# Performance work log

Measured on AMD Instinct MI355X. Metric: run time of the kernel, lower is better.

The kernel has to match this reference:

```python
import jax, jax.numpy as jnp
import numpy as np

DIM = 1024
HEADS = 16
DIM_HEAD = 64
INNER = HEADS * DIM_HEAD
SCALE = DIM_HEAD ** -0.5


def rotate_half(t):
    # '... (j d) -> ... j d' with j=2: split last dim in half
    x1, x2 = jnp.split(t, 2, axis=-1)
    return jnp.concatenate((-x2, x1), axis=-1)


def rotary_pos(n, d, dtype):
    inv_freq = 1.0 / (10000.0 ** (jnp.arange(0, d, 2, dtype=jnp.float32) / d))
    freqs = jnp.arange(n, dtype=jnp.float32)[:, None] * inv_freq[None, :]  # (n, d/2)
    return jnp.concatenate((freqs, freqs), axis=-1).astype(dtype)  # (n, d)


def apply_rope(pos, t):
    return t * jnp.cos(pos) + rotate_half(t) * jnp.sin(pos)


def setup_inputs() -> dict:
    key = jax.random.key(0)
    ks = jax.random.split(key, 5)
    x = jax.random.normal(ks[0], (2, 2048, DIM), dtype=jnp.float32)
    gamma = jnp.ones((DIM,), dtype=jnp.float32)
    beta = jnp.zeros((DIM,), dtype=jnp.float32)
    Wq = jax.random.normal(ks[1], (DIM, INNER), dtype=jnp.float32) * 0.02
    Wkv = jax.random.normal(ks[2], (DIM, 2 * INNER), dtype=jnp.float32) * 0.02
    Wo = jax.random.normal(ks[3], (INNER, DIM), dtype=jnp.float32) * 0.02
    return {"x": x, "gamma": gamma, "beta": beta, "Wq": Wq, "Wkv": Wkv, "Wo": Wo}


def reference(x, gamma, beta, Wq, Wkv, Wo):
    b, n, _ = x.shape
    # LayerNorm with learned gamma, fixed-zero beta buffer
    mu = jnp.mean(x, axis=-1, keepdims=True)
    var = jnp.var(x, axis=-1, keepdims=True)
    xn = (x - mu) / jnp.sqrt(var + 1e-5) * gamma + beta

    q = xn @ Wq                       # (b, n, inner)
    kv = xn @ Wkv
    k, v = jnp.split(kv, 2, axis=-1)

    def to_heads(t):
        return t.reshape(b, n, HEADS, DIM_HEAD).transpose(0, 2, 1, 3)  # b h n d

    q, k, v = map(to_heads, (q, k, v))

    pos = rotary_pos(n, DIM_HEAD, x.dtype)  # (n, d)
    q = apply_rope(pos, q)
    k = apply_rope(pos, k)

    q = q * SCALE
    sim = jnp.einsum('bhid,bhjd->bhij', q, k)

    neg = -jnp.finfo(sim.dtype).max
    causal_mask = jnp.triu(jnp.ones((n, n), dtype=bool), k=1)
    sim = jnp.where(causal_mask, neg, sim)

    attn = jax.nn.softmax(sim, axis=-1)
    out = jnp.einsum('bhij,bhjd->bhid', attn, v)
    out = out.transpose(0, 2, 1, 3).reshape(b, n, INNER)
    return out @ Wo
```

## Files before the change

kernel.cpp:

```cpp
#include <hip/hip_runtime.h>
#include <stdint.h>

typedef unsigned short u16;
typedef __attribute__((ext_vector_type(8))) short short8;
typedef __attribute__((ext_vector_type(4))) float floatx4;
typedef __attribute__((ext_vector_type(4))) unsigned short u16x4;
typedef __attribute__((ext_vector_type(2))) unsigned int uint2v;

__device__ __forceinline__ float bf2f(u16 v) {
  union { uint32_t u; float f; } x; x.u = ((uint32_t)v) << 16; return x.f;
}
__device__ __forceinline__ u16 f2bf(float f) {
  union { float f; uint32_t u; } x; x.f = f;
  uint32_t r = x.u + 0x7fffu + ((x.u >> 16) & 1u);
  return (u16)(r >> 16);
}
__device__ __forceinline__ uint32_t fu(float f) {
  union { float f; uint32_t u; } x; x.f = f; return x.u;
}

#define GL2LDS(g, l)                                                          \
  __builtin_amdgcn_global_load_lds(                                           \
      (const __attribute__((address_space(1))) void*)(g),                     \
      (__attribute__((address_space(3))) void*)(l), 16, 0, 0)

#define WAITBAR(N)                                                            \
  asm volatile("s_waitcnt vmcnt(" #N ")\n\ts_barrier" ::: "memory")

__global__ __launch_bounds__(256) void prep_k(const float* __restrict__ x,
                                              const float* __restrict__ gamma,
                                              const float* __restrict__ beta,
                                              const float* __restrict__ Wq,
                                              const float* __restrict__ Wkv,
                                              const float* __restrict__ Wo,
                                              u16* __restrict__ xn,
                                              u16* __restrict__ wqkvT,
                                              u16* __restrict__ woT) {
  int bid = blockIdx.x;
  int t = threadIdx.x;
  if (bid < 4096) {
    int row = bid;
    const float* xr = x + (size_t)row * 1024;
    float4 xv = *(const float4*)(xr + t * 4);
    float v0 = xv.x, v1 = xv.y, v2 = xv.z, v3 = xv.w;
    float s = v0 + v1 + v2 + v3;
    float s2 = v0 * v0 + v1 * v1 + v2 * v2 + v3 * v3;
#pragma unroll
    for (int d = 1; d < 64; d <<= 1) {
      s += __shfl_xor(s, d, 64);
      s2 += __shfl_xor(s2, d, 64);
    }
    __shared__ float red[8];
    int lane = t & 63, wv = t >> 6;
    if (lane == 0) { red[wv] = s; red[4 + wv] = s2; }
    __syncthreads();
    s = red[0] + red[1] + red[2] + red[3];
    s2 = red[4] + red[5] + red[6] + red[7];
    float mu = s * (1.0f / 1024.0f);
    float var = s2 * (1.0f / 1024.0f) - mu * mu;
    float rstd = rsqrtf(var + 1e-5f);
    float4 gv = *(const float4*)(gamma + t * 4);
    float4 bv = *(const float4*)(beta + t * 4);
    u16x4 ov;
    ov.x = f2bf((v0 - mu) * rstd * gv.x + bv.x);
    ov.y = f2bf((v1 - mu) * rstd * gv.y + bv.y);
    ov.z = f2bf((v2 - mu) * rstd * gv.z + bv.z);
    ov.w = f2bf((v3 - mu) * rstd * gv.w + bv.w);
    *(u16x4*)(xn + (size_t)row * 1024 + t * 4) = ov;
  } else {
    __shared__ float tile[32][33];
    int wb = bid - 4096;
    const float* in;
    u16* outp;
    int C;
    if (wb < 1024) { in = Wq; outp = wqkvT; C = 1024; }
    else if (wb < 3072) { wb -= 1024; in = Wkv; outp = wqkvT + 1024 * 1024; C = 2048; }
    else { wb -= 3072; in = Wo; outp = woT; C = 1024; }
    int nbx = C >> 5;
    int c0 = (wb % nbx) * 32, r0 = (wb / nbx) * 32;
    int tx = t & 31, ty = t >> 5;
#pragma unroll
    for (int i = 0; i < 32; i += 8)
      tile[ty + i][tx] = in[(size_t)(r0 + ty + i) * C + c0 + tx];
    __syncthreads();
#pragma unroll
    for (int i = 0; i < 32; i += 8)
      outp[(size_t)(c0 + ty + i) * 1024 + r0 + tx] = f2bf(tile[tx][ty + i]);
  }
}

__global__ __launch_bounds__(256) void gemm_qkv_k(const u16* __restrict__ A,
                                                  const u16* __restrict__ BT,
                                                  u16* __restrict__ C) {
  const int K = 1024, lda = 1024, ldc = 3072;
  __shared__ __align__(16) u16 lA[3][128 * 32];
  __shared__ __align__(16) u16 lB[3][128 * 32];
  int tid = threadIdx.x;
  int bm = blockIdx.y * 128;
  int bn = blockIdx.x * 128;
  int w = tid >> 6, l = tid & 63;
  int wm = (w >> 1) * 64, wn = (w & 1) * 64;
  int lr = l & 15, lq = l >> 4;
  floatx4 acc[4][4] = {};
  int sr = w * 16 + (l >> 2);
  int sc = (l & 3) * 8;
  int sds = sr * 32 + sc;
  const u16* pA0 = A + (size_t)(bm + sr) * lda + sc;
  const u16* pA1 = pA0 + (size_t)64 * lda;
  const u16* pB0 = BT + (size_t)(bn + sr) * K + sc;
  const u16* pB1 = pB0 + (size_t)64 * K;
  int ao[4], bo[4];
#pragma unroll
  for (int i = 0; i < 4; i++) {
    ao[i] = (wm + i * 16 + lr) * 32 + lq * 8;
    bo[i] = (wn + i * 16 + lr) * 32 + lq * 8;
  }

#define STAGE_QKV(bi)                                                         \
  {                                                                           \
    GL2LDS(pA0, &lA[bi][sds]);                                                \
    GL2LDS(pA1, &lA[bi][sds + 2048]);                                         \
    GL2LDS(pB0, &lB[bi][sds]);                                                \
    GL2LDS(pB1, &lB[bi][sds + 2048]);                                         \
    pA0 += 32; pA1 += 32; pB0 += 32; pB1 += 32;                               \
  }
#define COMPUTE_QKV(bi)                                                       \
  {                                                                           \
    short8 afr[4], bfr[4];                                                    \
    _Pragma("unroll") for (int i = 0; i < 4; i++)                             \
        afr[i] = *(const short8*)(&lA[bi][ao[i]]);                            \
    _Pragma("unroll") for (int i = 0; i < 4; i++)                             \
        bfr[i] = *(const short8*)(&lB[bi][bo[i]]);                            \
    _Pragma("unroll") for (int mi = 0; mi < 4; mi++)                          \
        _Pragma("unroll") for (int ni = 0; ni < 4; ni++)                      \
            acc[mi][ni] = __builtin_amdgcn_mfma_f32_16x16x32_bf16(            \
                afr[mi], bfr[ni], acc[mi][ni], 0, 0, 0);                      \
  }

  STAGE_QKV(0);
  STAGE_QKV(1);
#pragma unroll 1
  for (int t = 0; t < 10; ++t) {
    WAITBAR(4); STAGE_QKV(2); COMPUTE_QKV(0);
    WAITBAR(4); STAGE_QKV(0); COMPUTE_QKV(1);
    WAITBAR(4); STAGE_QKV(1); COMPUTE_QKV(2);
  }
  WAITBAR(4); COMPUTE_QKV(0);
  WAITBAR(0); COMPUTE_QKV(1);

  int sec = bn >> 10;
  if (sec == 2) {
#pragma unroll
    for (int mi = 0; mi < 4; mi++)
#pragma unroll
      for (int ni = 0; ni < 4; ni++) {
        int col = bn + wn + ni * 16 + lr;
        int cv = col - 2048;
        int row = bm + wm + mi * 16 + lq * 4;
        int bq = row >> 11;
        int n = row & 2047;
        int bh = (bq << 4) | (cv >> 6);
        int d = cv & 63;
        size_t L = ((size_t)(bh * 64 + d) << 11) + n;
        u16x4 ov;
        ov.x = f2bf(acc[mi][ni][0]);
        ov.y = f2bf(acc[mi][ni][1]);
        ov.z = f2bf(acc[mi][ni][2]);
        ov.w = f2bf(acc[mi][ni][3]);
        *(u16x4*)(C + (L >> 10) * 3072 + 2048 + (L & 1023)) = ov;
      }
  } else {
    float QS = (sec == 0) ? 0.125f * 1.44269504088896f : 1.0f;
#pragma unroll
    for (int ni = 0; ni < 2; ni++) {
      int i = ni * 16 + lr;
      float invf = exp2f(-(float)i * 0.4152410118609203f);
#pragma unroll
      for (int mi = 0; mi < 4; mi++)
#pragma unroll
        for (int r = 0; r < 4; r++) {
          int row = bm + wm + mi * 16 + lq * 4 + r;
          int n = row & 2047;
          float ang = (float)n * invf;
          float s_, c_;
          __sincosf(ang, &s_, &c_);
          float x1 = acc[mi][ni][r], x2 = acc[mi][ni + 2][r];
          int col = bn + wn + ni * 16 + lr;
          C[(size_t)row * ldc + col] = f2bf((x1 * c_ - x2 * s_) * QS);
          C[(size_t)row * ldc + col + 32] = f2bf((x2 * c_ + x1 * s_) * QS);
        }
    }
  }
}

__global__ __launch_bounds__(256) void gemm64_bf16_k(const u16* __restrict__ A,
                                                     const u16* __restrict__ BT,
                                                     float* __restrict__ C,
                                                     int K, int lda, int ldc) {
  __shared__ __align__(16) u16 lA[3][64 * 32];
  __shared__ __align__(16) u16 lB[3][128 * 32];
  int tid = threadIdx.x;
  int bm = blockIdx.y * 64;
  int bn = blockIdx.x * 128;
  int w = tid >> 6, l = tid & 63;
  int wm = (w >> 1) * 32, wn = (w & 1) * 64;
  int lr = l & 15, lq = l >> 4;
  floatx4 acc[2][4] = {};
  int sr = w * 16 + (l >> 2);
  int sc = (l & 3) * 8;
  int sds = sr * 32 + sc;
  const u16* pA0 = A + (size_t)(bm + sr) * lda + sc;
  const u16* pB0 = BT + (size_t)(bn + sr) * K + sc;
  const u16* pB1 = pB0 + (size_t)64 * K;
  int ao[2], bo[4];
#pragma unroll
  for (int i = 0; i < 2; i++) ao[i] = (wm + i * 16 + lr) * 32 + lq * 8;
#pragma unroll
  for (int i = 0; i < 4; i++) bo[i] = (wn + i * 16 + lr) * 32 + lq * 8;

#define STAGE_O(bi)                                                           \
  {                                                                           \
    GL2LDS(pA0, &lA[bi][sds]);                                                \
    GL2LDS(pB0, &lB[bi][sds]);                                                \
    GL2LDS(pB1, &lB[bi][sds + 2048]);                                         \
    pA0 += 32; pB0 += 32; pB1 += 32;                                          \
  }
#define COMPUTE_O(bi)                                                         \
  {                                                                           \
    short8 afr[2], bfr[4];                                                    \
    _Pragma("unroll") for (int i = 0; i < 2; i++)                             \
        afr[i] = *(const short8*)(&lA[bi][ao[i]]);                            \
    _Pragma("unroll") for (int i = 0; i < 4; i++)                             \
        bfr[i] = *(const short8*)(&lB[bi][bo[i]]);                            \
    _Pragma("unroll") for (int mi = 0; mi < 2; mi++)                          \
        _Pragma("unroll") for (int ni = 0; ni < 4; ni++)                      \
            acc[mi][ni] = __builtin_amdgcn_mfma_f32_16x16x32_bf16(            \
                afr[mi], bfr[ni], acc[mi][ni], 0, 0, 0);                      \
  }

  STAGE_O(0);
  STAGE_O(1);
#pragma unroll 1
  for (int t = 0; t < 10; ++t) {
    WAITBAR(3); STAGE_O(2); COMPUTE_O(0);
    WAITBAR(3); STAGE_O(0); COMPUTE_O(1);
    WAITBAR(3); STAGE_O(1); COMPUTE_O(2);
  }
  WAITBAR(3); COMPUTE_O(0);
  WAITBAR(0); COMPUTE_O(1);

#pragma unroll
  for (int mi = 0; mi < 2; mi++)
#pragma unroll
    for (int ni = 0; ni < 4; ni++)
#pragma unroll
      for (int r = 0; r < 4; r++) {
        int row = bm + wm + mi * 16 + lq * 4 + r;
        int col = bn + wn + ni * 16 + lr;
        C[(size_t)row * ldc + col] = acc[mi][ni][r];
      }
}

#define LPT 64
#define FIXM 4.0f
__device__ __forceinline__ void attn_tile2(const u16* lK, const u16* lV, u16* lp,
                                           const short8* aq, floatx4* o,
                                           float& l_i, int lr, int lq,
                                           bool diag, int q0, int k0g,
                                           short8 ones) {
  floatx4 s[4];
#pragma unroll
  for (int ni = 0; ni < 4; ni++) {
    floatx4 a = {};
#pragma unroll
    for (int kc = 0; kc < 2; kc++) {
      int R = ni * 16 + lr;
      int c8 = (kc * 4 + lq) ^ (R & 7);
      short8 kf = *(const short8*)&lK[R * 64 + c8 * 8];
      a = __builtin_amdgcn_mfma_f32_16x16x32_bf16(kf, aq[kc], a, 0, 0, 0);
    }
    s[ni] = a;
  }
  if (diag) {
    int qg = q0 + lr;
#pragma unroll
    for (int ni = 0; ni < 4; ni++)
#pragma unroll
      for (int r = 0; r < 4; r++) {
        int kg = k0g + ni * 16 + lq * 4 + r;
        if (kg > qg) s[ni][r] = -1e30f;
      }
  }
  int swz = (lr & 7) << 3;
#pragma unroll
  for (int ni = 0; ni < 4; ni++) {
    float p0 = exp2f(s[ni][0] - FIXM), p1 = exp2f(s[ni][1] - FIXM);
    float p2 = exp2f(s[ni][2] - FIXM), p3 = exp2f(s[ni][3] - FIXM);
    uint2v dw;
    dw.x = __builtin_amdgcn_perm(fu(p1), fu(p0), 0x07060302u);
    dw.y = __builtin_amdgcn_perm(fu(p3), fu(p2), 0x07060302u);
    *(uint2v*)&lp[lr * LPT + ((ni * 16 + lq * 4) ^ swz)] = dw;
  }
  short8 pb0 = *(const short8*)&lp[lr * LPT + ((lq * 8) ^ swz)];
  short8 pb1 = *(const short8*)&lp[lr * LPT + ((32 + lq * 8) ^ swz)];
  floatx4 z = {};
  z = __builtin_amdgcn_mfma_f32_16x16x32_bf16(ones, pb0, z, 0, 0, 0);
  z = __builtin_amdgcn_mfma_f32_16x16x32_bf16(ones, pb1, z, 0, 0, 0);
  l_i += z[0];
#pragma unroll
  for (int di = 0; di < 4; di++) {
    int R = di * 16 + lr;
    int c80 = lq ^ (R & 7);
    int c81 = (4 + lq) ^ (R & 7);
    short8 v0 = *(const short8*)&lV[R * 64 + c80 * 8];
    o[di] = __builtin_amdgcn_mfma_f32_16x16x32_bf16(v0, pb0, o[di], 0, 0, 0);
    short8 v1 = *(const short8*)&lV[R * 64 + c81 * 8];
    o[di] = __builtin_amdgcn_mfma_f32_16x16x32_bf16(v1, pb1, o[di], 0, 0, 0);
  }
}

__global__ __launch_bounds__(256) void attn_k(const u16* __restrict__ qkv,
                                              u16* __restrict__ out) {
  __shared__ __align__(16) u16 lK[2][64 * 64];
  __shared__ __align__(16) u16 lV[2][64 * 64];
  __shared__ __align__(16) u16 lP[4][16 * LPT];
  int bh = blockIdx.x;
  int b = bh >> 4, h = bh & 15;
  int y = blockIdx.y;
  int g = y >> 3, o_ = y & 7;
  int j = (g & 1) ? ((g << 3) + 7 - o_) : y;
  int tid = threadIdx.x;
  int w = tid >> 6, l = tid & 63;
  int lr = l & 15, lq = l >> 4;
  int q0 = j * 64 + w * 16;
  const u16* qb = qkv + (size_t)b * 2048 * 3072 + h * 64;
  const u16* kb = qkv + (size_t)b * 2048 * 3072 + 1024 + h * 64;
  int bh64 = bh * 64;
  short8 aq[2];
  aq[0] = *(const short8*)(qb + (size_t)(q0 + lr) * 3072 + lq * 8);
  aq[1] = *(const short8*)(qb + (size_t)(q0 + lr) * 3072 + 32 + lq * 8);
  short8 ones;
#pragma unroll
  for (int i = 0; i < 8; i++) ones[i] = (short)0x3F80;
  floatx4 o[4] = {};
  float l_ = 0.0f;
  int srow8 = l >> 3;
  int sc8 = (l & 7) ^ srow8;
  u16* lp = &lP[w][0];
  auto stage = [&](int bufi, int kt) {
#pragma unroll
    for (int c = 0; c < 2; c++) {
      int m = w + c * 4;
      int row = m * 8 + srow8;
      GL2LDS(kb + (size_t)(kt * 64 + row) * 3072 + sc8 * 8, &lK[bufi][m * 512]);
      int nn = kt * 64 + sc8 * 8;
      GL2LDS(qkv + (size_t)((bh64 + row) * 2 + (nn >> 10)) * 3072 + 2048 +
                 (nn & 1023),
             &lV[bufi][m * 512]);
    }
  };
  stage(0, 0);
  for (int kt = 0; kt <= j; ++kt) {
    int cur = kt & 1;
    __syncthreads();
    if (kt < j) stage(cur ^ 1, kt + 1);
    attn_tile2(lK[cur], lV[cur], lp, aq, o, l_, lr, lq, kt == j, q0, kt * 64,
               ones);
  }
  float rl = 1.0f / l_;
#pragma unroll
  for (int di = 0; di < 4; di++) {
    uint2v dw;
    u16 a0 = f2bf(o[di][0] * rl), a1 = f2bf(o[di][1] * rl);
    u16 a2 = f2bf(o[di][2] * rl), a3 = f2bf(o[di][3] * rl);
    dw.x = (uint32_t)a0 | ((uint32_t)a1 << 16);
    dw.y = (uint32_t)a2 | ((uint32_t)a3 << 16);
    int dcol = h * 64 + di * 16 + lq * 4;
    *(uint2v*)(out + ((size_t)(b * 2048 + q0 + lr)) * 1024 + dcol) = dw;
  }
}

extern "C" void kernel_launch(void* const* d_in, const int* in_sizes, int n_in,
                              void* d_out, int out_size, void* d_ws, size_t ws_size,
                              hipStream_t stream) {
  const float* x = (const float*)d_in[0];
  const float* gamma = (const float*)d_in[1];
  const float* beta = (const float*)d_in[2];
  const float* Wq = (const float*)d_in[3];
  const float* Wkv = (const float*)d_in[4];
  const float* Wo = (const float*)d_in[5];
  float* out = (float*)d_out;
  char* ws = (char*)d_ws;

  u16* qkv = (u16*)(ws);
  u16* wqkvT = (u16*)(ws + 25165824);
  u16* woT = (u16*)(ws + 31457280);
  u16* xn = (u16*)(ws + 33554432);
  u16* attn_out = xn;

  prep_k<<<8192, 256, 0, stream>>>(x, gamma, beta, Wq, Wkv, Wo, xn, wqkvT, woT);
  gemm_qkv_k<<<dim3(24, 32), 256, 0, stream>>>(xn, wqkvT, qkv);
  attn_k<<<dim3(32, 32), 256, 0, stream>>>(qkv, attn_out);
  gemm64_bf16_k<<<dim3(8, 64), 256, 0, stream>>>(attn_out, woT, out, 1024, 1024, 1024);
}
```

Measured before the change: 196.1 us.

## Retile QKV GEMM to 128x384 with 512 threads and load V directly to registers

```diff
diff --git a/kernel.cpp b/kernel.cpp
--- a/kernel.cpp
+++ b/kernel.cpp
@@ -26,6 +26,8 @@
 
 #define WAITBAR(N)                                                            \
   asm volatile("s_waitcnt vmcnt(" #N ")\n\ts_barrier" ::: "memory")
+#define BARX asm volatile("s_barrier" ::: "memory")
+#define VM0BARX asm volatile("s_waitcnt vmcnt(0)\n\ts_barrier" ::: "memory")
 
 __global__ __launch_bounds__(256) void prep_k(const float* __restrict__ x,
                                               const float* __restrict__ gamma,
@@ -89,106 +91,125 @@
   }
 }
 
-__global__ __launch_bounds__(256) void gemm_qkv_k(const u16* __restrict__ A,
-                                                  const u16* __restrict__ BT,
-                                                  u16* __restrict__ C) {
-  const int K = 1024, lda = 1024, ldc = 3072;
-  __shared__ __align__(16) u16 lA[3][128 * 32];
-  __shared__ __align__(16) u16 lB[3][128 * 32];
+__global__ __launch_bounds__(512, 1) void gemm_qkv_k(const u16* __restrict__ A,
+                                                     const u16* __restrict__ BT,
+                                                     u16* __restrict__ C) {
+  __shared__ __align__(16) u16 sA[2][128 * 64];
+  __shared__ __align__(16) u16 sB[2][384 * 64];
   int tid = threadIdx.x;
+  int w = tid >> 6, l = tid & 63;
+  int lr = l & 15, lq = l >> 4;
+  int wm = w >> 1, wn = w & 1;
   int bm = blockIdx.y * 128;
-  int bn = blockIdx.x * 128;
-  int w = tid >> 6, l = tid & 63;
-  int wm = (w >> 1) * 64, wn = (w & 1) * 64;
-  int lr = l & 15, lq = l >> 4;
-  floatx4 acc[4][4] = {};
-  int sr = w * 16 + (l >> 2);
-  int sc = (l & 3) * 8;
-  int sds = sr * 32 + sc;
-  const u16* pA0 = A + (size_t)(bm + sr) * lda + sc;
-  const u16* pA1 = pA0 + (size_t)64 * lda;
-  const u16* pB0 = BT + (size_t)(bn + sr) * K + sc;
-  const u16* pB1 = pB0 + (size_t)64 * K;
-  int ao[4], bo[4];
-#pragma unroll
-  for (int i = 0; i < 4; i++) {
-    ao[i] = (wm + i * 16 + lr) * 32 + lq * 8;
-    bo[i] = (wn + i * 16 + lr) * 32 + lq * 8;
-  }
-
-#define STAGE_QKV(bi)                                                         \
+  int bn = blockIdx.x * 384;
+  floatx4 acc[2][12] = {};
+  int gcol = ((tid & 7) ^ ((tid >> 3) & 7)) * 8;
+  int strow = tid >> 3;
+  int t8 = tid * 8;
+  const u16* gA = A + (size_t)(bm + strow) * 1024 + gcol;
+  const u16* gB = BT + (size_t)(bn + strow) * 1024 + gcol;
+  int csw = (lr & 7) << 3;
+  int ar = (wm * 32 + lr) * 64;
+  int br = (wn * 192 + lr) * 64;
+
+#define ST_A(bi)                                                              \
+  { GL2LDS(gA, &sA[bi][t8]); GL2LDS(gA + 65536, &sA[bi][t8 + 4096]); }
+#define ST_B(bi)                                                              \
+  { GL2LDS(gB, &sB[bi][t8]);                                                  \
+    GL2LDS(gB + 65536, &sB[bi][t8 + 4096]);                                   \
+    GL2LDS(gB + 131072, &sB[bi][t8 + 8192]);                                  \
+    GL2LDS(gB + 196608, &sB[bi][t8 + 12288]);                                 \
+    GL2LDS(gB + 262144, &sB[bi][t8 + 16384]);                                 \
+    GL2LDS(gB + 327680, &sB[bi][t8 + 20480]); }
+#define HALF(p, kh)                                                           \
   {                                                                           \
-    GL2LDS(pA0, &lA[bi][sds]);                                                \
-    GL2LDS(pA1, &lA[bi][sds + 2048]);                                         \
-    GL2LDS(pB0, &lB[bi][sds]);                                                \
-    GL2LDS(pB1, &lB[bi][sds + 2048]);                                         \
-    pA0 += 32; pA1 += 32; pB0 += 32; pB1 += 32;                               \
-  }
-#define COMPUTE_QKV(bi)                                                       \
+    int co_ = ((kh)*32 + lq * 8) ^ csw;                                       \
+    short8 a0_ = *(const short8*)&sA[p][ar + co_];                            \
+    short8 a1_ = *(const short8*)&sA[p][ar + 1024 + co_];                     \
+    _Pragma("unroll") for (int g = 0; g < 3; g++) {                           \
+      short8 b0_ = *(const short8*)&sB[p][br + (g * 4 + 0) * 1024 + co_];     \
+      short8 b1_ = *(const short8*)&sB[p][br + (g * 4 + 1) * 1024 + co_];     \
+      short8 b2_ = *(const short8*)&sB[p][br + (g * 4 + 2) * 1024 + co_];     \
+      short8 b3_ = *(const short8*)&sB[p][br + (g * 4 + 3) * 1024 + co_];     \
+      acc[0][g*4+0] = __builtin_amdgcn_mfma_f32_16x16x32_bf16(a0_, b0_, acc[0][g*4+0], 0, 0, 0); \
+      acc[1][g*4+0] = __builtin_amdgcn_mfma_f32_16x16x32_bf16(a1_, b0_, acc[1][g*4+0], 0, 0, 0); \
+      acc[0][g*4+1] = __builtin_amdgcn_mfma_f32_16x16x32_bf16(a0_, b1_, acc[0][g*4+1], 0, 0, 0); \
+      acc[1][g*4+1] = __builtin_amdgcn_mfma_f32_16x16x32_bf16(a1_, b1_, acc[1][g*4+1], 0, 0, 0); \
+      acc[0][g*4+2] = __builtin_amdgcn_mfma_f32_16x16x32_bf16(a0_, b2_, acc[0][g*4+2], 0, 0, 0); \
+      acc[1][g*4+2] = __builtin_amdgcn_mfma_f32_16x16x32_bf16(a1_, b2_, acc[1][g*4+2], 0, 0, 0); \
+      acc[0][g*4+3] = __builtin_amdgcn_mfma_f32_16x16x32_bf16(a0_, b3_, acc[0][g*4+3], 0, 0, 0); \
+      acc[1][g*4+3] = __builtin_amdgcn_mfma_f32_16x16x32_bf16(a1_, b3_, acc[1][g*4+3], 0, 0, 0); \
+    }                                                                         \
+  }
+#define KT(p, q, DOST)                                                        \
   {                                                                           \
-    short8 afr[4], bfr[4];                                                    \
-    _Pragma("unroll") for (int i = 0; i < 4; i++)                             \
-        afr[i] = *(const short8*)(&lA[bi][ao[i]]);                            \
-    _Pragma("unroll") for (int i = 0; i < 4; i++)                             \
-        bfr[i] = *(const short8*)(&lB[bi][bo[i]]);                            \
-    _Pragma("unroll") for (int mi = 0; mi < 4; mi++)                          \
-        _Pragma("unroll") for (int ni = 0; ni < 4; ni++)                      \
-            acc[mi][ni] = __builtin_amdgcn_mfma_f32_16x16x32_bf16(            \
-                afr[mi], bfr[ni], acc[mi][ni], 0, 0, 0);                      \
-  }
-
-  STAGE_QKV(0);
-  STAGE_QKV(1);
+    if (DOST) { ST_A(q); ST_B(q); gA += 64; gB += 64; }                       \
+    BARX; __builtin_amdgcn_s_setprio(1);                                      \
+    HALF(p, 0);                                                               \
+    __builtin_amdgcn_s_setprio(0); BARX;                                      \
+    __builtin_amdgcn_s_setprio(1);                                            \
+    HALF(p, 1);                                                               \
+    __builtin_amdgcn_s_setprio(0); VM0BARX;                                   \
+  }
+
+  ST_A(0); ST_B(0); gA += 64; gB += 64;
+  VM0BARX;
 #pragma unroll 1
-  for (int t = 0; t < 10; ++t) {
-    WAITBAR(4); STAGE_QKV(2); COMPUTE_QKV(0);
-    WAITBAR(4); STAGE_QKV(0); COMPUTE_QKV(1);
-    WAITBAR(4); STAGE_QKV(1); COMPUTE_QKV(2);
-  }
-  WAITBAR(4); COMPUTE_QKV(0);
-  WAITBAR(0); COMPUTE_QKV(1);
-
-  int sec = bn >> 10;
-  if (sec == 2) {
-#pragma unroll
-    for (int mi = 0; mi < 4; mi++)
-#pragma unroll
-      for (int ni = 0; ni < 4; ni++) {
-        int col = bn + wn + ni * 16 + lr;
+  for (int t = 0; t < 7; ++t) {
+    KT(0, 1, 1);
+    KT(1, 0, 1);
+  }
+  KT(0, 1, 1);
+  KT(1, 0, 0);
+
+#pragma unroll
+  for (int nig = 0; nig < 3; nig++) {
+    int col0 = bn + wn * 192 + nig * 64;
+    int sec = col0 >> 10;
+    if (sec == 2) {
+#pragma unroll
+      for (int p4 = 0; p4 < 4; p4++) {
+        int ni = nig * 4 + p4;
+        int col = col0 + p4 * 16 + lr;
         int cv = col - 2048;
-        int row = bm + wm + mi * 16 + lq * 4;
-        int bq = row >> 11;
-        int n = row & 2047;
-        int bh = (bq << 4) | (cv >> 6);
-        int d = cv & 63;
-        size_t L = ((size_t)(bh * 64 + d) << 11) + n;
-        u16x4 ov;
-        ov.x = f2bf(acc[mi][ni][0]);
-        ov.y = f2bf(acc[mi][ni][1]);
-        ov.z = f2bf(acc[mi][ni][2]);
-        ov.w = f2bf(acc[mi][ni][3]);
-        *(u16x4*)(C + (L >> 10) * 3072 + 2048 + (L & 1023)) = ov;
+#pragma unroll
+        for (int mi = 0; mi < 2; mi++) {
+          int row = bm + wm * 32 + mi * 16 + lq * 4;
+          int bq = row >> 11;
+          int n = row & 2047;
+          int bh = (bq << 4) | (cv >> 6);
+          int d = cv & 63;
+          size_t L = ((size_t)(bh * 64 + d) << 11) + n;
+          u16x4 ov;
+          ov.x = f2bf(acc[mi][ni][0]);
+          ov.y = f2bf(acc[mi][ni][1]);
+          ov.z = f2bf(acc[mi][ni][2]);
+          ov.w = f2bf(acc[mi][ni][3]);
+          *(u16x4*)(C + (L >> 10) * 3072 + 2048 + (L & 1023)) = ov;
+        }
       }
-  } else {
-    float QS = (sec == 0) ? 0.125f * 1.44269504088896f : 1.0f;
-#pragma unroll
-    for (int ni = 0; ni < 2; ni++) {
-      int i = ni * 16 + lr;
-      float invf = exp2f(-(float)i * 0.4152410118609203f);
-#pragma unroll
-      for (int mi = 0; mi < 4; mi++)
-#pragma unroll
-        for (int r = 0; r < 4; r++) {
-          int row = bm + wm + mi * 16 + lq * 4 + r;
-          int n = row & 2047;
-          float ang = (float)n * invf;
-          float s_, c_;
-          __sincosf(ang, &s_, &c_);
-          float x1 = acc[mi][ni][r], x2 = acc[mi][ni + 2][r];
-          int col = bn + wn + ni * 16 + lr;
-          C[(size_t)row * ldc + col] = f2bf((x1 * c_ - x2 * s_) * QS);
-          C[(size_t)row * ldc + col + 32] = f2bf((x2 * c_ + x1 * s_) * QS);
-        }
+    } else {
+      float QS = (sec == 0) ? 0.125f * 1.44269504088896f : 1.0f;
+#pragma unroll
+      for (int np = 0; np < 2; np++) {
+        int i = np * 16 + lr;
+        float invf = exp2f(-(float)i * 0.4152410118609203f);
+#pragma unroll
+        for (int mi = 0; mi < 2; mi++)
+#pragma unroll
+          for (int r = 0; r < 4; r++) {
+            int row = bm + wm * 32 + mi * 16 + lq * 4 + r;
+            int n = row & 2047;
+            float ang = (float)n * invf;
+            float s_, c_;
+            __sincosf(ang, &s_, &c_);
+            float x1 = acc[mi][nig * 4 + np][r];
+            float x2 = acc[mi][nig * 4 + np + 2][r];
+            int col = col0 + np * 16 + lr;
+            C[(size_t)row * 3072 + col] = f2bf((x1 * c_ - x2 * s_) * QS);
+            C[(size_t)row * 3072 + col + 32] = f2bf((x2 * c_ + x1 * s_) * QS);
+          }
+      }
     }
   }
 }
@@ -262,9 +283,9 @@
 }
 
 #define LPT 64
-#define FIXM 4.0f
-__device__ __forceinline__ void attn_tile2(const u16* lK, const u16* lV, u16* lp,
-                                           const short8* aq, floatx4* o,
+__device__ __forceinline__ void attn_stepR(const u16* lK, u16* lp,
+                                           const short8* aq,
+                                           const short8 (&vv)[4][2], floatx4* o,
                                            float& l_i, int lr, int lq,
                                            bool diag, int q0, int k0g,
                                            short8 ones) {
@@ -294,8 +315,8 @@
   int swz = (lr & 7) << 3;
 #pragma unroll
   for (int ni = 0; ni < 4; ni++) {
-    float p0 = exp2f(s[ni][0] - FIXM), p1 = exp2f(s[ni][1] - FIXM);
-    float p2 = exp2f(s[ni][2] - FIXM), p3 = exp2f(s[ni][3] - FIXM);
+    float p0 = exp2f(s[ni][0]), p1 = exp2f(s[ni][1]);
+    float p2 = exp2f(s[ni][2]), p3 = exp2f(s[ni][3]);
     uint2v dw;
     dw.x = __builtin_amdgcn_perm(fu(p1), fu(p0), 0x07060302u);
     dw.y = __builtin_amdgcn_perm(fu(p3), fu(p2), 0x07060302u);
@@ -309,20 +330,14 @@
   l_i += z[0];
 #pragma unroll
   for (int di = 0; di < 4; di++) {
-    int R = di * 16 + lr;
-    int c80 = lq ^ (R & 7);
-    int c81 = (4 + lq) ^ (R & 7);
-    short8 v0 = *(const short8*)&lV[R * 64 + c80 * 8];
-    o[di] = __builtin_amdgcn_mfma_f32_16x16x32_bf16(v0, pb0, o[di], 0, 0, 0);
-    short8 v1 = *(const short8*)&lV[R * 64 + c81 * 8];
-    o[di] = __builtin_amdgcn_mfma_f32_16x16x32_bf16(v1, pb1, o[di], 0, 0, 0);
-  }
-}
-
-__global__ __launch_bounds__(256) void attn_k(const u16* __restrict__ qkv,
-                                              u16* __restrict__ out) {
+    o[di] = __builtin_amdgcn_mfma_f32_16x16x32_bf16(vv[di][0], pb0, o[di], 0, 0, 0);
+    o[di] = __builtin_amdgcn_mfma_f32_16x16x32_bf16(vv[di][1], pb1, o[di], 0, 0, 0);
+  }
+}
+
+__global__ __launch_bounds__(256, 4) void attn_k(const u16* __restrict__ qkv,
+                                                 u16* __restrict__ out) {
   __shared__ __align__(16) u16 lK[2][64 * 64];
-  __shared__ __align__(16) u16 lV[2][64 * 64];
   __shared__ __align__(16) u16 lP[4][16 * LPT];
   int bh = blockIdx.x;
   int b = bh >> 4, h = bh & 15;
@@ -347,25 +362,40 @@
   int srow8 = l >> 3;
   int sc8 = (l & 7) ^ srow8;
   u16* lp = &lP[w][0];
-  auto stage = [&](int bufi, int kt) {
+  auto stageK = [&](int bufi, int kt) {
 #pragma unroll
     for (int c = 0; c < 2; c++) {
       int m = w + c * 4;
       int row = m * 8 + srow8;
       GL2LDS(kb + (size_t)(kt * 64 + row) * 3072 + sc8 * 8, &lK[bufi][m * 512]);
-      int nn = kt * 64 + sc8 * 8;
-      GL2LDS(qkv + (size_t)((bh64 + row) * 2 + (nn >> 10)) * 3072 + 2048 +
-                 (nn & 1023),
-             &lV[bufi][m * 512]);
     }
   };
-  stage(0, 0);
-  for (int kt = 0; kt <= j; ++kt) {
-    int cur = kt & 1;
+  auto loadV = [&](short8 (&dst)[4][2], int kt) {
+#pragma unroll
+    for (int di = 0; di < 4; di++) {
+      int d = di * 16 + lr;
+      const u16* p_ = qkv +
+                      ((size_t)((bh64 + d) * 2 + (kt >> 4))) * 3072 + 2048 +
+                      (kt & 15) * 64 + lq * 8;
+      dst[di][0] = *(const short8*)p_;
+      dst[di][1] = *(const short8*)(p_ + 32);
+    }
+  };
+  short8 vA[4][2], vB[4][2];
+  stageK(0, 0);
+  loadV(vA, 0);
+  int kt = 0, cur = 0;
+  while (true) {
     __syncthreads();
-    if (kt < j) stage(cur ^ 1, kt + 1);
-    attn_tile2(lK[cur], lV[cur], lp, aq, o, l_, lr, lq, kt == j, q0, kt * 64,
-               ones);
+    if (kt < j) { stageK(cur ^ 1, kt + 1); loadV(vB, kt + 1); }
+    attn_stepR(lK[cur], lp, aq, vA, o, l_, lr, lq, kt == j, q0, kt * 64, ones);
+    if (kt == j) break;
+    ++kt; cur ^= 1;
+    __syncthreads();
+    if (kt < j) { stageK(cur ^ 1, kt + 1); loadV(vA, kt + 1); }
+    attn_stepR(lK[cur], lp, aq, vB, o, l_, lr, lq, kt == j, q0, kt * 64, ones);
+    if (kt == j) break;
+    ++kt; cur ^= 1;
   }
   float rl = 1.0f / l_;
 #pragma unroll
@@ -399,7 +429,7 @@
   u16* attn_out = xn;
 
   prep_k<<<8192, 256, 0, stream>>>(x, gamma, beta, Wq, Wkv, Wo, xn, wqkvT, woT);
-  gemm_qkv_k<<<dim3(24, 32), 256, 0, stream>>>(xn, wqkvT, qkv);
+  gemm_qkv_k<<<dim3(8, 32), 512, 0, stream>>>(xn, wqkvT, qkv);
   attn_k<<<dim3(32, 32), 256, 0, stream>>>(qkv, attn_out);
   gemm64_bf16_k<<<dim3(8, 64), 256, 0, stream>>>(attn_out, woT, out, 1024, 1024, 1024);
 }
```

Result: slower. 222.0 us (+13.2%).
